# Kernel tuning notes

Measured on AMD Instinct MI355X. Metric: run time of the kernel, lower is better.

Reference implementation:

```python
import jax, jax.numpy as jnp
import numpy as np
import math

B, L, D, H = 4, 1024, 512, 8
TAU = 0.1
LN_EPS = 1e-5


def _attn(xq, xk, xv, wq, bq, wk, bk, wv, bv, wo, bo, energy=None, threshold=None):
    Bq, Lq, Dm = xq.shape
    Dh = Dm // H
    Q = (xq @ wq.T + bq).reshape(Bq, Lq, H, Dh)
    K = (xk @ wk.T + bk).reshape(Bq, -1, H, Dh)
    V = (xv @ wv.T + bv).reshape(Bq, -1, H, Dh)
    sc = jnp.einsum('bqhd,bkhd->bhqk', Q, K) / jnp.sqrt(jnp.float32(Dh))
    if energy is not None:
        # mask keys whose mean |energy| over channels is below threshold
        mask = jnp.abs(energy).mean(-1)[:, None, None, :] > threshold  # (B,1,1,Lk)
        sc = jnp.where(mask, sc, -jnp.inf)
    w = jnp.nan_to_num(jax.nn.softmax(sc, axis=-1))  # nan->0 for fully-masked rows
    o = jnp.einsum('bhqk,bkhd->bqhd', w, V).reshape(Bq, Lq, Dm)
    return o @ wo.T + bo


def _ln(x, w, b):
    m = x.mean(-1, keepdims=True)
    v = x.var(-1, keepdims=True)
    return (x - m) / jnp.sqrt(v + LN_EPS) * w + b


def _mlp(x, w1, b1, w2, b2):
    h = jax.nn.gelu(x @ w1.T + b1, approximate=False)  # torch nn.GELU default = exact
    return h @ w2.T + b2


def setup_inputs():
    key = jax.random.key(0)
    ks = list(jax.random.split(key, 64))

    def nxt():
        return ks.pop(0)

    def w(shape, scale=0.02):
        return jax.random.normal(nxt(), shape, dtype=jnp.float32) * scale

    inp = {
        'LL': jax.random.normal(nxt(), (B, D, L), dtype=jnp.float32),
        'LH': jax.random.normal(nxt(), (B, D, L), dtype=jnp.float32),
        'raw_tau': jnp.float32(math.log(TAU / (1.0 - TAU))),
    }
    for p in ('llA', 'lhA', 'crA'):
        for nm in ('q', 'k', 'v', 'o'):
            inp[f'{p}_w{nm}'] = w((D, D))
            inp[f'{p}_b{nm}'] = jnp.zeros((D,), jnp.float32)
    for p in ('mlp_ll', 'mlp_lh'):
        inp[f'{p}_w1'] = w((4 * D, D))
        inp[f'{p}_b1'] = jnp.zeros((4 * D,), jnp.float32)
        inp[f'{p}_w2'] = w((D, 4 * D))
        inp[f'{p}_b2'] = jnp.zeros((D,), jnp.float32)
    inp['n1_w'] = jnp.ones((D,), jnp.float32)
    inp['n1_b'] = jnp.zeros((D,), jnp.float32)
    inp['n2_w'] = jnp.ones((D,), jnp.float32)
    inp['n2_b'] = jnp.zeros((D,), jnp.float32)
    return inp


def reference(LL, LH, raw_tau,
              llA_wq, llA_bq, llA_wk, llA_bk, llA_wv, llA_bv, llA_wo, llA_bo,
              lhA_wq, lhA_bq, lhA_wk, lhA_bk, lhA_wv, lhA_bv, lhA_wo, lhA_bo,
              crA_wq, crA_bq, crA_wk, crA_bk, crA_wv, crA_bv, crA_wo, crA_bo,
              mlp_ll_w1, mlp_ll_b1, mlp_ll_w2, mlp_ll_b2,
              mlp_lh_w1, mlp_lh_b1, mlp_lh_w2, mlp_lh_b2,
              n1_w, n1_b, n2_w, n2_b):
    tau = jax.nn.sigmoid(raw_tau)
    ll_s = jnp.transpose(LL, (0, 2, 1))  # (B,L,D)
    lh_s = jnp.transpose(LH, (0, 2, 1))
    ll_o = _attn(ll_s, ll_s, ll_s, llA_wq, llA_bq, llA_wk, llA_bk, llA_wv, llA_bv, llA_wo, llA_bo)
    lh_o = _attn(lh_s, lh_s, lh_s, lhA_wq, lhA_bq, lhA_wk, lhA_bk, lhA_wv, lhA_bv, lhA_wo, lhA_bo,
                 energy=lh_s, threshold=tau)
    cr_o = _attn(ll_o, lh_o, lh_o, crA_wq, crA_bq, crA_wk, crA_bk, crA_wv, crA_bv, crA_wo, crA_bo)
    ll_f = _ln(ll_s + ll_o + cr_o, n1_w, n1_b)
    ll_f = _mlp(ll_f, mlp_ll_w1, mlp_ll_b1, mlp_ll_w2, mlp_ll_b2) + ll_f
    lh_f = _ln(lh_s + lh_o, n2_w, n2_b)
    lh_f = _mlp(lh_f, mlp_lh_w1, mlp_lh_b1, mlp_lh_w2, mlp_lh_b2) + lh_f
    return (jnp.transpose(ll_f, (0, 2, 1)), jnp.transpose(lh_f, (0, 2, 1)))
```

## Files before the change

### kernel.cpp

```cpp
#include <hip/hip_runtime.h>
#include <hip/hip_bf16.h>
#include <stdint.h>

typedef unsigned short u16;
typedef __bf16 bf16_t;
typedef bf16_t bf16x8 __attribute__((ext_vector_type(8)));
typedef float f32x4 __attribute__((ext_vector_type(4)));

#define DEV static __device__ __forceinline__

DEV u16 f2b(float f) {
    __hip_bfloat16 h = __float2bfloat16(f);
    return __builtin_bit_cast(u16, h);
}

DEV bf16x8 ld_frag(const u16* p) {
    uint4 u = *reinterpret_cast<const uint4*>(p);
    return __builtin_bit_cast(bf16x8, u);
}

DEV float gelu(float v) {
    float y = 0.79788456080286536f * (v + 0.044715f * v * v * v);
    float e = __expf(-2.f * fabsf(y));
    float th = (1.f - e) / (1.f + e);
    th = copysignf(th, y);
    return 0.5f * v * (1.f + th);
}

DEV void gl_lds16(const u16* g, u16* l) {
    __builtin_amdgcn_global_load_lds(
        (const __attribute__((address_space(1))) void*)(uintptr_t)g,
        (__attribute__((address_space(3))) void*)(unsigned int)(uintptr_t)l,
        16, 0, 0);
}

struct ConvEnt { const float* s; u16* d; int n; };
struct ConvArgs { ConvEnt e[16]; };

__global__ __launch_bounds__(256) void k_conv(ConvArgs a) {
    const ConvEnt en = a.e[blockIdx.y];
    for (int i = (blockIdx.x * 256 + threadIdx.x) * 4; i < en.n; i += 256 * 256 * 4) {
        const float4 f = *reinterpret_cast<const float4*>(en.s + i);
        unsigned r0 = (unsigned)f2b(f.x) | ((unsigned)f2b(f.y) << 16);
        unsigned r1 = (unsigned)f2b(f.z) | ((unsigned)f2b(f.w) << 16);
        uint2 rr; rr.x = r0; rr.y = r1;
        *reinterpret_cast<uint2*>(en.d + i) = rr;
    }
}

struct CpyEnt { const float* s; float* d; };
struct CpyArgs { CpyEnt e[8]; };

__global__ __launch_bounds__(256) void k_cpyf(CpyArgs a) {
    const CpyEnt en = a.e[blockIdx.y];
    int i = blockIdx.x * 256 + threadIdx.x;
    en.d[i] = en.s[i];
}

__global__ __launch_bounds__(256) void k_tin(const float* __restrict__ LL, const float* __restrict__ LH,
                                             float* __restrict__ llf, u16* __restrict__ llb,
                                             float* __restrict__ lhf, u16* __restrict__ lhb) {
    __shared__ float t[32][33];
    int z = blockIdx.z, b = z & 3;
    const float* in = (z < 4) ? LL : LH;
    float* of = (z < 4) ? llf : lhf;
    u16* ob = (z < 4) ? llb : lhb;
    int l0 = blockIdx.x * 32, d0 = blockIdx.y * 32;
    int tx = threadIdx.x, ty = threadIdx.y;
#pragma unroll
    for (int j = 0; j < 4; ++j) {
        int d = d0 + ty + j * 8;
        t[ty + j * 8][tx] = in[((size_t)b * 512 + d) * 1024 + l0 + tx];
    }
    __syncthreads();
#pragma unroll
    for (int j = 0; j < 4; ++j) {
        int l = l0 + ty + j * 8;
        float v = t[tx][ty + j * 8];
        size_t o = ((size_t)b * 1024 + l) * 512 + d0 + tx;
        of[o] = v;
        ob[o] = f2b(v);
    }
}

__global__ __launch_bounds__(256) void k_tout(const float* __restrict__ y0, const float* __restrict__ y1,
                                              float* __restrict__ out) {
    __shared__ float t[32][33];
    int z = blockIdx.z, b = z & 3;
    const float* in = (z < 4) ? y0 : y1;
    float* o = out + ((z < 4) ? 0 : (size_t)4096 * 512);
    int l0 = blockIdx.x * 32, d0 = blockIdx.y * 32;
    int tx = threadIdx.x, ty = threadIdx.y;
#pragma unroll
    for (int j = 0; j < 4; ++j) {
        int l = l0 + ty + j * 8;
        t[ty + j * 8][tx] = in[((size_t)b * 1024 + l) * 512 + d0 + tx];
    }
    __syncthreads();
#pragma unroll
    for (int j = 0; j < 4; ++j) {
        int d = d0 + ty + j * 8;
        o[((size_t)b * 512 + d) * 1024 + l0 + tx] = t[tx][ty + j * 8];
    }
}

__global__ __launch_bounds__(256) void k_mask(const float* __restrict__ lh_s,
                                              const float* __restrict__ raw_tau,
                                              float* __restrict__ kbias) {
    int row = blockIdx.x * 4 + (threadIdx.x >> 6);
    int lane = threadIdx.x & 63;
    const float* p = lh_s + (size_t)row * 512 + lane * 8;
    float s = 0.f;
#pragma unroll
    for (int j = 0; j < 8; ++j) s += fabsf(p[j]);
#pragma unroll
    for (int m = 32; m >= 1; m >>= 1) s += __shfl_xor(s, m, 64);
    float tau = 1.f / (1.f + expf(-raw_tau[0]));
    if (lane == 0) kbias[row] = (s * (1.f / 512.f) > tau) ? 0.f : -3.0e38f;
}

__global__ __launch_bounds__(256) void k_ln(const float* __restrict__ a, const float* __restrict__ b,
                                            const float* __restrict__ c, const float* __restrict__ w,
                                            const float* __restrict__ bi,
                                            float* __restrict__ of, u16* __restrict__ ob) {
    int row = blockIdx.x * 4 + (threadIdx.x >> 6);
    int lane = threadIdx.x & 63;
    size_t base = (size_t)row * 512 + lane * 8;
    float x[8];
#pragma unroll
    for (int j = 0; j < 8; ++j) {
        float v = a[base + j] + b[base + j];
        if (c) v += c[base + j];
        x[j] = v;
    }
    float s = 0.f, s2 = 0.f;
#pragma unroll
    for (int j = 0; j < 8; ++j) { s += x[j]; s2 += x[j] * x[j]; }
#pragma unroll
    for (int m = 32; m >= 1; m >>= 1) { s += __shfl_xor(s, m, 64); s2 += __shfl_xor(s2, m, 64); }
    float mean = s * (1.f / 512.f);
    float var = s2 * (1.f / 512.f) - mean * mean;
    float rs = rsqrtf(var + 1e-5f);
#pragma unroll
    for (int j = 0; j < 8; ++j) {
        float y = (x[j] - mean) * rs * w[lane * 8 + j] + bi[lane * 8 + j];
        of[base + j] = y;
        ob[base + j] = f2b(y);
    }
}

struct GP {
    const u16* A; const u16* W; const float* bias; const float* res;
    float* Cf; u16* Cb; u16* Qp; u16* Kp; u16* Vt;
    int N, K, kB, vB, nwg;
};

template <int BM, int BN, int GELU_ACT, int PACK>
__global__ __launch_bounds__(256) void k_gemm(GP p0, GP p1, int M) {
    constexpr int BK = 64;
    __shared__ alignas(16) u16 Al[2][BM * BK];
    __shared__ alignas(16) u16 Wl[2][BN * BK];
    GP g = (blockIdx.y == 0) ? p0 : p1;
    const int orig = blockIdx.x;
    if (orig >= g.nwg) return;
    int bid;
    {
        const int xcd = orig & 7, lin = orig >> 3;
        const int q = g.nwg >> 3, r = g.nwg & 7;
        bid = (xcd < r ? xcd * (q + 1) : r * (q + 1) + (xcd - r) * q) + lin;
    }
    const int K = g.K, N = g.N;
    const int nny = N / BN;
    const int m0 = (bid / nny) * BM, n0 = (bid % nny) * BN;

    const int t = threadIdx.x, w = t >> 6, l = t & 63;
    constexpr int FM = BM / 32, FN = BN / 32;
    const int wr = w >> 1, wc = w & 1;
    const int lq = l & 15, lg = l >> 4;
    f32x4 acc[FM][FN] = {};

    const int srow = l >> 3, schunk = l & 7;
    auto stage = [&](int kcol, int buf) {
#pragma unroll
        for (int i = 0; i < BM / 32; ++i) {
            const int row = i * 32 + w * 8 + srow;
            gl_lds16(g.A + (size_t)(m0 + row) * K + kcol + ((schunk ^ (row & 7)) * 8),
                     &Al[buf][(i * 32 + w * 8) * BK]);
        }
#pragma unroll
        for (int i = 0; i < BN / 32; ++i) {
            const int row = i * 32 + w * 8 + srow;
            gl_lds16(g.W + (size_t)(n0 + row) * K + kcol + ((schunk ^ (row & 7)) * 8),
                     &Wl[buf][(i * 32 + w * 8) * BK]);
        }
    };

    stage(0, 0);
    const int KT = K / BK;
    for (int kt = 0; kt < KT; ++kt) {
        const int cur = kt & 1;
        __syncthreads();
        if (kt + 1 < KT) stage((kt + 1) * BK, cur ^ 1);
#pragma unroll
        for (int s = 0; s < 2; ++s) {
            bf16x8 af[FM], bw[FN];
#pragma unroll
            for (int i = 0; i < FM; ++i) {
                const int row = wr * (BM / 2) + i * 16 + lq;
                af[i] = ld_frag(&Al[cur][row * BK + (((s * 4 + lg) ^ (row & 7)) * 8)]);
            }
#pragma unroll
            for (int j = 0; j < FN; ++j) {
                const int row = wc * (BN / 2) + j * 16 + lq;
                bw[j] = ld_frag(&Wl[cur][row * BK + (((s * 4 + lg) ^ (row & 7)) * 8)]);
            }
#pragma unroll
            for (int i = 0; i < FM; ++i)
#pragma unroll
                for (int j = 0; j < FN; ++j)
                    acc[i][j] = __builtin_amdgcn_mfma_f32_16x16x32_bf16(af[i], bw[j], acc[i][j], 0, 0, 0);
        }
    }

    if (PACK && n0 >= g.vB) {
        u16* T = (u16*)Al;
        constexpr int CH = BM / 8, CMASK = CH - 1, SH = (CH == 16) ? 4 : 3;
        __syncthreads();
#pragma unroll
        for (int i = 0; i < FM; ++i) {
#pragma unroll
            for (int j = 0; j < FN; ++j) {
                const int ni = wc * (BN / 2) + j * 16 + lq;
                const float bn = g.bias[n0 + ni];
#pragma unroll
                for (int r2 = 0; r2 < 4; ++r2) {
                    const int mi = wr * (BM / 2) + i * 16 + lg * 4 + r2;
                    T[ni * BM + (((mi >> 3) ^ (ni & CMASK)) * 8) + (mi & 7)] = f2b(acc[i][j][r2] + bn);
                }
            }
        }
        __syncthreads();
        const int bb = m0 >> 10, mloc = m0 & 1023;
        const int mc = t & CMASK, nib = t >> SH;
        constexpr int RPP = 256 / CH;
#pragma unroll
        for (int p2 = 0; p2 < BN / RPP; ++p2) {
            const int ni = nib + p2 * RPP;
            uint4 u = *reinterpret_cast<const uint4*>(&T[ni * BM + ((mc ^ (ni & CMASK)) * 8)]);
            const int d = n0 - g.vB + ni;
            *reinterpret_cast<uint4*>(
                &g.Vt[((size_t)(bb * 8 + (d >> 6)) * 64 + (d & 63)) * 1024 + mloc + mc * 8]) = u;
        }
        return;
    }

#pragma unroll
    for (int i = 0; i < FM; ++i) {
#pragma unroll
        for (int j = 0; j < FN; ++j) {
            const int n = n0 + wc * (BN / 2) + j * 16 + lq;
            const float bn = g.bias[n];
#pragma unroll
            for (int r2 = 0; r2 < 4; ++r2) {
                const int m = m0 + wr * (BM / 2) + i * 16 + lg * 4 + r2;
                float v = acc[i][j][r2] + bn;
                if (GELU_ACT) v = gelu(v);
                if (PACK) {
                    const int bb = m >> 10, ll_ = m & 1023;
                    if (n >= g.kB) {
                        const int d = n - g.kB;
                        g.Kp[((size_t)(bb * 8 + (d >> 6)) * 1024 + ll_) * 64 + (d & 63)] = f2b(v);
                    } else {
                        g.Qp[((size_t)(bb * 8 + (n >> 6)) * 1024 + ll_) * 64 + (n & 63)] = f2b(v * 0.125f);
                    }
                } else {
                    size_t o = (size_t)m * N + n;
                    if (g.res) v += g.res[o];
                    if (g.Cf) g.Cf[o] = v;
                    if (g.Cb) g.Cb[o] = f2b(v);
                }
            }
        }
    }
}

__global__ __launch_bounds__(256) void k_attn(const u16* __restrict__ Qp, const u16* __restrict__ Kp,
                                              const u16* __restrict__ Vtp, u16* __restrict__ O,
                                              const float* __restrict__ kbias, int nwg) {
    constexpr int L = 1024;
    __shared__ alignas(16) u16 Kl[2][64 * 64];
    __shared__ alignas(16) u16 Vl[2][64 * 64];
    __shared__ alignas(16) u16 Pl[64 * 64];
    const int t = threadIdx.x, w = t >> 6, l = t & 63;
    int bid;
    {
        const int orig = blockIdx.x;
        bid = (orig & 7) * (nwg >> 3) + (orig >> 3);
    }
    const int bh = bid >> 4, q0 = (bid & 15) * 64;
    const int bz = bh >> 3, h = bh & 7;
    const int lq = l & 15, lg = l >> 4;
    const float* kb = (kbias != nullptr && bz >= 4) ? (kbias + (size_t)(bz - 4) * L) : nullptr;

    bf16x8 qa0, qa1;
    {
        const u16* qp = Qp + ((size_t)bh * L + q0 + w * 16 + lq) * 64 + lg * 8;
        qa0 = ld_frag(qp);
        qa1 = ld_frag(qp + 32);
    }

    const int r0 = w * 16 + (l >> 3), r1 = r0 + 8, c = l & 7;
    const u16* Ksrc0 = Kp + (size_t)bh * L * 64 + (size_t)r0 * 64 + ((c ^ (r0 & 7)) * 8);
    const u16* Ksrc1 = Kp + (size_t)bh * L * 64 + (size_t)r1 * 64 + ((c ^ (r1 & 7)) * 8);
    const u16* Vsrc0 = Vtp + (size_t)bh * 64 * L + (size_t)r0 * L + ((c ^ (r0 & 7)) * 8);
    const u16* Vsrc1 = Vtp + (size_t)bh * 64 * L + (size_t)r1 * L + ((c ^ (r1 & 7)) * 8);

    auto stage = [&](int k0, int buf) {
        gl_lds16(Ksrc0 + (size_t)k0 * 64, &Kl[buf][(w * 16) * 64]);
        gl_lds16(Ksrc1 + (size_t)k0 * 64, &Kl[buf][(w * 16 + 8) * 64]);
        gl_lds16(Vsrc0 + k0, &Vl[buf][(w * 16) * 64]);
        gl_lds16(Vsrc1 + k0, &Vl[buf][(w * 16 + 8) * 64]);
    };

    int addrA[4][2];
#pragma unroll
    for (int f = 0; f < 4; ++f) {
        int row = f * 16 + lq;
#pragma unroll
        for (int s = 0; s < 2; ++s) addrA[f][s] = row * 64 + (((s * 4 + lg) ^ (row & 7)) * 8);
    }
    const int paddr0 = (w * 16 + lq) * 64 + ((lg ^ (lq & 7)) * 8);
    const int paddr1 = (w * 16 + lq) * 64 + (((4 + lg) ^ (lq & 7)) * 8);

    f32x4 oacc[4] = {};
    float lrow[4] = {0.f, 0.f, 0.f, 0.f};

    stage(0, 0);
    for (int kt = 0; kt < 16; ++kt) {
        const int cur = kt & 1;
        __syncthreads();
        if (kt + 1 < 16) stage((kt + 1) * 64, cur ^ 1);

        f32x4 sc4[4];
#pragma unroll
        for (int f = 0; f < 4; ++f) {
            f32x4 a = {};
            a = __builtin_amdgcn_mfma_f32_16x16x32_bf16(qa0, ld_frag(&Kl[cur][addrA[f][0]]), a, 0, 0, 0);
            a = __builtin_amdgcn_mfma_f32_16x16x32_bf16(qa1, ld_frag(&Kl[cur][addrA[f][1]]), a, 0, 0, 0);
            sc4[f] = a;
        }
#pragma unroll
        for (int f = 0; f < 4; ++f) {
            float bv = kb ? kb[kt * 64 + f * 16 + lq] : 0.f;
#pragma unroll
            for (int r = 0; r < 4; ++r) {
                float pv = __expf(sc4[f][r] + bv);
                lrow[r] += pv;
                const int prow = w * 16 + lg * 4 + r;
                Pl[prow * 64 + (((f * 2 + (lq >> 3)) ^ (prow & 7)) * 8) + (lq & 7)] = f2b(pv);
            }
        }
        bf16x8 pa0 = ld_frag(&Pl[paddr0]);
        bf16x8 pa1 = ld_frag(&Pl[paddr1]);
#pragma unroll
        for (int db = 0; db < 4; ++db) {
            oacc[db] = __builtin_amdgcn_mfma_f32_16x16x32_bf16(pa0, ld_frag(&Vl[cur][addrA[db][0]]), oacc[db], 0, 0, 0);
            oacc[db] = __builtin_amdgcn_mfma_f32_16x16x32_bf16(pa1, ld_frag(&Vl[cur][addrA[db][1]]), oacc[db], 0, 0, 0);
        }
    }
#pragma unroll
    for (int r = 0; r < 4; ++r) {
        float v = lrow[r];
#pragma unroll
        for (int msk = 8; msk >= 1; msk >>= 1) v += __shfl_xor(v, msk, 16);
        lrow[r] = v;
    }
#pragma unroll
    for (int db = 0; db < 4; ++db) {
#pragma unroll
        for (int r = 0; r < 4; ++r) {
            float denom = lrow[r];
            float v = (denom > 0.f) ? oacc[db][r] / denom : 0.f;
            O[((size_t)bz * L + q0 + w * 16 + lg * 4 + r) * 512 + h * 64 + db * 16 + lq] = f2b(v);
        }
    }
}

extern "C" void kernel_launch(void* const* d_in, const int* in_sizes, int n_in,
                              void* d_out, int out_size, void* d_ws, size_t ws_size,
                              hipStream_t stream) {
    const int M = 4096;
    const float* LL = (const float*)d_in[0];
    const float* LH = (const float*)d_in[1];
    const float* raw_tau = (const float*)d_in[2];
    auto F = [&](int i) { return (const float*)d_in[i]; };
    const int BIG = 1 << 28;

    char* p = (char*)d_ws;
    auto alloc = [&](size_t bytes) { void* r = (void*)p; p += (bytes + 255) & ~(size_t)255; return r; };
    const size_t MDf = (size_t)M * 512 * 4, MDb = (size_t)M * 512 * 2;
    float* ll_s_f = (float*)alloc(MDf);
    float* lh_s_f = (float*)alloc(MDf);
    u16* ll_s_b = (u16*)alloc(MDb);
    u16* lh_s_b = (u16*)alloc(MDb);
    u16* Qp = (u16*)alloc(2 * MDb);
    u16* Kp = (u16*)alloc(2 * MDb);
    u16* Vt = (u16*)alloc(2 * MDb);
    u16* Cxb = (u16*)alloc(2 * MDb);
    float* ll_o_f = (float*)alloc(MDf);
    u16* ll_o_b = (u16*)alloc(MDb);
    float* lh_o_f = (float*)alloc(MDf);
    u16* lh_o_b = (u16*)alloc(MDb);
    float* cr_o_f = (float*)alloc(MDf);
    float* ln_f_ll = (float*)alloc(MDf);
    float* ln_f_lh = (float*)alloc(MDf);
    u16* ln_b = (u16*)alloc(MDb);
    u16* hb = (u16*)alloc((size_t)M * 2048 * 2);
    float* yf_ll = (float*)alloc(MDf);
    float* yf_lh = (float*)alloc(MDf);
    float* kbias = (float*)alloc(4096 * 4);
    float* bqkv_ll = (float*)alloc(1536 * 4);
    float* bqkv_lh = (float*)alloc(1536 * 4);
    float* bkv_cr = (float*)alloc(1024 * 4);
    const size_t WDD = (size_t)262144;
    u16* wqkv_ll = (u16*)alloc(3 * WDD * 2);
    u16* wqkv_lh = (u16*)alloc(3 * WDD * 2);
    u16* wkv_cr = (u16*)alloc(2 * WDD * 2);
    u16* wq_cr = (u16*)alloc(WDD * 2);
    u16* wo_ll = (u16*)alloc(WDD * 2);
    u16* wo_lh = (u16*)alloc(WDD * 2);
    u16* wo_cr = (u16*)alloc(WDD * 2);
    u16* wm[4];
    for (int i = 0; i < 4; ++i) wm[i] = (u16*)alloc((size_t)1048576 * 2);

    const size_t SET = (size_t)4 * 8 * 1024 * 64;

    ConvArgs ca;
    ca.e[0] = {F(3), wqkv_ll, (int)WDD};
    ca.e[1] = {F(5), wqkv_ll + WDD, (int)WDD};
    ca.e[2] = {F(7), wqkv_ll + 2 * WDD, (int)WDD};
    ca.e[3] = {F(11), wqkv_lh, (int)WDD};
    ca.e[4] = {F(13), wqkv_lh + WDD, (int)WDD};
    ca.e[5] = {F(15), wqkv_lh + 2 * WDD, (int)WDD};
    ca.e[6] = {F(19), wq_cr, (int)WDD};
    ca.e[7] = {F(21), wkv_cr, (int)WDD};
    ca.e[8] = {F(23), wkv_cr + WDD, (int)WDD};
    ca.e[9] = {F(9), wo_ll, (int)WDD};
    ca.e[10] = {F(17), wo_lh, (int)WDD};
    ca.e[11] = {F(25), wo_cr, (int)WDD};
    ca.e[12] = {F(27), wm[0], 1048576};
    ca.e[13] = {F(29), wm[1], 1048576};
    ca.e[14] = {F(31), wm[2], 1048576};
    ca.e[15] = {F(33), wm[3], 1048576};
    k_conv<<<dim3(256, 16), 256, 0, stream>>>(ca);

    CpyArgs cp;
    cp.e[0] = {F(4), bqkv_ll};
    cp.e[1] = {F(6), bqkv_ll + 512};
    cp.e[2] = {F(8), bqkv_ll + 1024};
    cp.e[3] = {F(12), bqkv_lh};
    cp.e[4] = {F(14), bqkv_lh + 512};
    cp.e[5] = {F(16), bqkv_lh + 1024};
    cp.e[6] = {F(22), bkv_cr};
    cp.e[7] = {F(24), bkv_cr + 512};
    k_cpyf<<<dim3(2, 8), 256, 0, stream>>>(cp);

    k_tin<<<dim3(32, 16, 8), dim3(32, 8), 0, stream>>>(LL, LH, ll_s_f, ll_s_b, lh_s_f, lh_s_b);
    k_mask<<<dim3(1024), 256, 0, stream>>>(lh_s_f, raw_tau, kbias);

    auto gp = [&](const u16* A, const u16* W, const float* bias, int N, int K, int nwg) {
        GP g = {};
        g.A = A; g.W = W; g.bias = bias; g.N = N; g.K = K; g.nwg = nwg;
        g.kB = BIG; g.vB = BIG;
        return g;
    };

    {
        GP a = gp(ll_s_b, wqkv_ll, bqkv_ll, 1536, 512, 384);
        a.kB = 512; a.vB = 1024; a.Qp = Qp; a.Kp = Kp; a.Vt = Vt;
        GP b = gp(lh_s_b, wqkv_lh, bqkv_lh, 1536, 512, 384);
        b.kB = 512; b.vB = 1024; b.Qp = Qp + SET; b.Kp = Kp + SET; b.Vt = Vt + SET;
        k_gemm<128, 128, 0, 1><<<dim3(384, 2), 256, 0, stream>>>(a, b, M);
    }
    k_attn<<<dim3(1024), 256, 0, stream>>>(Qp, Kp, Vt, Cxb, kbias, 1024);
    {
        GP a = gp(Cxb, wo_ll, F(10), 512, 512, 512);
        a.Cf = ll_o_f; a.Cb = ll_o_b;
        GP b = gp(Cxb + SET, wo_lh, F(18), 512, 512, 512);
        b.Cf = lh_o_f; b.Cb = lh_o_b;
        k_gemm<64, 64, 0, 0><<<dim3(512, 2), 256, 0, stream>>>(a, b, M);
    }
    k_ln<<<dim3(1024), 256, 0, stream>>>(lh_s_f, lh_o_f, nullptr, F(37), F(38), ln_f_lh, ln_b);
    {
        GP a = gp(ln_b, wm[2], F(32), 2048, 512, 512);
        a.Cb = hb;
        k_gemm<128, 128, 1, 0><<<dim3(512, 1), 256, 0, stream>>>(a, a, M);
    }
    {
        GP a = gp(ll_o_b, wq_cr, F(20), 512, 512, 512);
        a.Qp = Qp;
        GP b = gp(lh_o_b, wkv_cr, bkv_cr, 1024, 512, 1024);
        b.kB = 0; b.vB = 512; b.Kp = Kp; b.Vt = Vt;
        k_gemm<64, 64, 0, 1><<<dim3(1024, 2), 256, 0, stream>>>(a, b, M);
    }
    k_attn<<<dim3(512), 256, 0, stream>>>(Qp, Kp, Vt, Cxb, nullptr, 512);
    {
        GP a = gp(Cxb, wo_cr, F(26), 512, 512, 512);
        a.Cf = cr_o_f;
        GP b = gp(hb, wm[3], F(34), 512, 2048, 512);
        b.Cf = yf_lh; b.res = ln_f_lh;
        k_gemm<64, 64, 0, 0><<<dim3(512, 2), 256, 0, stream>>>(a, b, M);
    }
    k_ln<<<dim3(1024), 256, 0, stream>>>(ll_s_f, ll_o_f, cr_o_f, F(35), F(36), ln_f_ll, ln_b);
    {
        GP a = gp(ln_b, wm[0], F(28), 2048, 512, 512);
        a.Cb = hb;
        k_gemm<128, 128, 1, 0><<<dim3(512, 1), 256, 0, stream>>>(a, a, M);
    }
    {
        GP a = gp(hb, wm[1], F(30), 512, 2048, 512);
        a.Cf = yf_ll; a.res = ln_f_ll;
        k_gemm<64, 64, 0, 0><<<dim3(512, 1), 256, 0, stream>>>(a, a, M);
    }
    k_tout<<<dim3(32, 16, 8), dim3(32, 8), 0, stream>>>(yf_ll, yf_lh, (float*)d_out);
}
```

Baseline: 273.9 us.

## Process 128 queries per attention workgroup to reuse K/V tiles

The attention kernel now handles a 128-query tile per workgroup, with each wave computing two 16-row query fragments instead of one. Each K and V fragment loaded from LDS feeds two MFMAs, and each staged K/V tile is shared across twice as many queries, which halves global K/V traffic. The grid sizes are halved to match. In exchange, register use and the LDS P buffer double. The cross-attention launch drops to 256 workgroups, which may underfill the GPU's compute units.

Result: no change. 268.7 us (-1.9%).

```diff
diff --git a/kernel.cpp b/kernel.cpp
--- a/kernel.cpp
+++ b/kernel.cpp
@@ -290,23 +290,20 @@
     constexpr int L = 1024;
     __shared__ alignas(16) u16 Kl[2][64 * 64];
     __shared__ alignas(16) u16 Vl[2][64 * 64];
-    __shared__ alignas(16) u16 Pl[64 * 64];
+    __shared__ alignas(16) u16 Pl[128 * 64];
     const int t = threadIdx.x, w = t >> 6, l = t & 63;
-    int bid;
-    {
-        const int orig = blockIdx.x;
-        bid = (orig & 7) * (nwg >> 3) + (orig >> 3);
-    }
-    const int bh = bid >> 4, q0 = (bid & 15) * 64;
+    const int bid = ((int)blockIdx.x & 7) * (nwg >> 3) + ((int)blockIdx.x >> 3);
+    const int bh = bid >> 3, q0 = (bid & 7) * 128;
     const int bz = bh >> 3, h = bh & 7;
     const int lq = l & 15, lg = l >> 4;
     const float* kb = (kbias != nullptr && bz >= 4) ? (kbias + (size_t)(bz - 4) * L) : nullptr;
 
-    bf16x8 qa0, qa1;
-    {
-        const u16* qp = Qp + ((size_t)bh * L + q0 + w * 16 + lq) * 64 + lg * 8;
-        qa0 = ld_frag(qp);
-        qa1 = ld_frag(qp + 32);
+    bf16x8 qa[2][2];
+#pragma unroll
+    for (int i = 0; i < 2; ++i) {
+        const u16* qp = Qp + ((size_t)bh * L + q0 + w * 32 + i * 16 + lq) * 64 + lg * 8;
+        qa[i][0] = ld_frag(qp);
+        qa[i][1] = ld_frag(qp + 32);
     }
 
     const int r0 = w * 16 + (l >> 3), r1 = r0 + 8, c = l & 7;
@@ -329,11 +326,17 @@
 #pragma unroll
         for (int s = 0; s < 2; ++s) addrA[f][s] = row * 64 + (((s * 4 + lg) ^ (row & 7)) * 8);
     }
-    const int paddr0 = (w * 16 + lq) * 64 + ((lg ^ (lq & 7)) * 8);
-    const int paddr1 = (w * 16 + lq) * 64 + (((4 + lg) ^ (lq & 7)) * 8);
-
-    f32x4 oacc[4] = {};
-    float lrow[4] = {0.f, 0.f, 0.f, 0.f};
+    int paddr[2][2], pwbase[2];
+#pragma unroll
+    for (int i = 0; i < 2; ++i) {
+        const int prow = w * 32 + i * 16 + lq;
+#pragma unroll
+        for (int s = 0; s < 2; ++s) paddr[i][s] = prow * 64 + (((s * 4 + lg) ^ (prow & 7)) * 8);
+        pwbase[i] = w * 32 + i * 16 + lg * 4;
+    }
+
+    f32x4 oacc[2][4] = {};
+    float lrow[2][4] = {};
 
     stage(0, 0);
     for (int kt = 0; kt < 16; ++kt) {
@@ -341,47 +344,69 @@
         __syncthreads();
         if (kt + 1 < 16) stage((kt + 1) * 64, cur ^ 1);
 
-        f32x4 sc4[4];
+        f32x4 sc[2][4];
 #pragma unroll
         for (int f = 0; f < 4; ++f) {
-            f32x4 a = {};
-            a = __builtin_amdgcn_mfma_f32_16x16x32_bf16(qa0, ld_frag(&Kl[cur][addrA[f][0]]), a, 0, 0, 0);
-            a = __builtin_amdgcn_mfma_f32_16x16x32_bf16(qa1, ld_frag(&Kl[cur][addrA[f][1]]), a, 0, 0, 0);
-            sc4[f] = a;
+            bf16x8 k0 = ld_frag(&Kl[cur][addrA[f][0]]);
+            bf16x8 k1 = ld_frag(&Kl[cur][addrA[f][1]]);
+#pragma unroll
+            for (int i = 0; i < 2; ++i) {
+                f32x4 a = {};
+                a = __builtin_amdgcn_mfma_f32_16x16x32_bf16(qa[i][0], k0, a, 0, 0, 0);
+                a = __builtin_amdgcn_mfma_f32_16x16x32_bf16(qa[i][1], k1, a, 0, 0, 0);
+                sc[i][f] = a;
+            }
         }
 #pragma unroll
         for (int f = 0; f < 4; ++f) {
             float bv = kb ? kb[kt * 64 + f * 16 + lq] : 0.f;
 #pragma unroll
+            for (int i = 0; i < 2; ++i) {
+#pragma unroll
+                for (int r = 0; r < 4; ++r) {
+                    float pv = __expf(sc[i][f][r] + bv);
+                    lrow[i][r] += pv;
+                    const int prow = pwbase[i] + r;
+                    Pl[prow * 64 + (((f * 2 + (lq >> 3)) ^ (prow & 7)) * 8) + (lq & 7)] = f2b(pv);
+                }
+            }
+        }
+        bf16x8 pa[2][2];
+#pragma unroll
+        for (int i = 0; i < 2; ++i) {
+            pa[i][0] = ld_frag(&Pl[paddr[i][0]]);
+            pa[i][1] = ld_frag(&Pl[paddr[i][1]]);
+        }
+#pragma unroll
+        for (int db = 0; db < 4; ++db) {
+            bf16x8 v0 = ld_frag(&Vl[cur][addrA[db][0]]);
+            bf16x8 v1 = ld_frag(&Vl[cur][addrA[db][1]]);
+#pragma unroll
+            for (int i = 0; i < 2; ++i) {
+                oacc[i][db] = __builtin_amdgcn_mfma_f32_16x16x32_bf16(pa[i][0], v0, oacc[i][db], 0, 0, 0);
+                oacc[i][db] = __builtin_amdgcn_mfma_f32_16x16x32_bf16(pa[i][1], v1, oacc[i][db], 0, 0, 0);
+            }
+        }
+    }
+#pragma unroll
+    for (int i = 0; i < 2; ++i)
+#pragma unroll
+        for (int r = 0; r < 4; ++r) {
+            float v = lrow[i][r];
+#pragma unroll
+            for (int msk = 8; msk >= 1; msk >>= 1) v += __shfl_xor(v, msk, 16);
+            lrow[i][r] = v;
+        }
+#pragma unroll
+    for (int i = 0; i < 2; ++i) {
+#pragma unroll
+        for (int db = 0; db < 4; ++db) {
+#pragma unroll
             for (int r = 0; r < 4; ++r) {
-                float pv = __expf(sc4[f][r] + bv);
-                lrow[r] += pv;
-                const int prow = w * 16 + lg * 4 + r;
-                Pl[prow * 64 + (((f * 2 + (lq >> 3)) ^ (prow & 7)) * 8) + (lq & 7)] = f2b(pv);
-            }
-        }
-        bf16x8 pa0 = ld_frag(&Pl[paddr0]);
-        bf16x8 pa1 = ld_frag(&Pl[paddr1]);
-#pragma unroll
-        for (int db = 0; db < 4; ++db) {
-            oacc[db] = __builtin_amdgcn_mfma_f32_16x16x32_bf16(pa0, ld_frag(&Vl[cur][addrA[db][0]]), oacc[db], 0, 0, 0);
-            oacc[db] = __builtin_amdgcn_mfma_f32_16x16x32_bf16(pa1, ld_frag(&Vl[cur][addrA[db][1]]), oacc[db], 0, 0, 0);
-        }
-    }
-#pragma unroll
-    for (int r = 0; r < 4; ++r) {
-        float v = lrow[r];
-#pragma unroll
-        for (int msk = 8; msk >= 1; msk >>= 1) v += __shfl_xor(v, msk, 16);
-        lrow[r] = v;
-    }
-#pragma unroll
-    for (int db = 0; db < 4; ++db) {
-#pragma unroll
-        for (int r = 0; r < 4; ++r) {
-            float denom = lrow[r];
-            float v = (denom > 0.f) ? oacc[db][r] / denom : 0.f;
-            O[((size_t)bz * L + q0 + w * 16 + lg * 4 + r) * 512 + h * 64 + db * 16 + lq] = f2b(v);
+                float denom = lrow[i][r];
+                float v = (denom > 0.f) ? oacc[i][db][r] / denom : 0.f;
+                O[((size_t)bz * L + q0 + w * 32 + i * 16 + lg * 4 + r) * 512 + h * 64 + db * 16 + lq] = f2b(v);
+            }
         }
     }
 }
@@ -482,7 +507,7 @@
         b.kB = 512; b.vB = 1024; b.Qp = Qp + SET; b.Kp = Kp + SET; b.Vt = Vt + SET;
         k_gemm<128, 128, 0, 1><<<dim3(384, 2), 256, 0, stream>>>(a, b, M);
     }
-    k_attn<<<dim3(1024), 256, 0, stream>>>(Qp, Kp, Vt, Cxb, kbias, 1024);
+    k_attn<<<dim3(512), 256, 0, stream>>>(Qp, Kp, Vt, Cxb, kbias, 512);
     {
         GP a = gp(Cxb, wo_ll, F(10), 512, 512, 512);
         a.Cf = ll_o_f; a.Cb = ll_o_b;
@@ -503,7 +528,7 @@
         b.kB = 0; b.vB = 512; b.Kp = Kp; b.Vt = Vt;
         k_gemm<64, 64, 0, 1><<<dim3(1024, 2), 256, 0, stream>>>(a, b, M);
     }
-    k_attn<<<dim3(512), 256, 0, stream>>>(Qp, Kp, Vt, Cxb, nullptr, 512);
+    k_attn<<<dim3(256), 256, 0, stream>>>(Qp, Kp, Vt, Cxb, nullptr, 256);
     {
         GP a = gp(Cxb, wo_cr, F(26), 512, 512, 512);
         a.Cf = cr_o_f;
```
